# Kernel optimization log

Measured on AMD Instinct MI355X. Metric: run time of the kernel, lower is better.

Reference implementation:

```python
import jax, jax.numpy as jnp
import numpy as np

GS = 8        # grid_size
MARGIN = 1.0
LAMBDA = 1.0
BIG = 5.0     # mask penalty added to similarity matrix


def _bilinear(desc, coords):
    # desc: (c,h,w); coords: (n,2) as (y,x) in descriptor pixel space
    c, h, w = desc.shape
    y = jnp.clip(coords[:, 0], 0.0, h - 1.0)
    x = jnp.clip(coords[:, 1], 0.0, w - 1.0)
    y0 = jnp.floor(y); x0 = jnp.floor(x)
    y1 = jnp.minimum(y0 + 1.0, h - 1.0)
    x1 = jnp.minimum(x0 + 1.0, w - 1.0)
    wy = y - y0; wx = x - x0
    y0i = y0.astype(jnp.int32); y1i = y1.astype(jnp.int32)
    x0i = x0.astype(jnp.int32); x1i = x1.astype(jnp.int32)
    v00 = desc[:, y0i, x0i]; v01 = desc[:, y0i, x1i]
    v10 = desc[:, y1i, x0i]; v11 = desc[:, y1i, x1i]
    out = (v00 * (1 - wy) * (1 - wx) + v01 * (1 - wy) * wx
           + v10 * wy * (1 - wx) + v11 * wy * wx)
    return out.T  # (n,c)


def _forward(desc1, desc2, homo12, w_vis_mask1, score2):
    b, cdim, hc, wc = desc1.shape
    flat = hc * wc
    H, W = score2.shape[2], score2.shape[3]
    dt = desc1.dtype

    gy, gx = jnp.meshgrid(jnp.arange(hc, dtype=dt), jnp.arange(wc, dtype=dt), indexing='ij')
    # corner coordinate grid in image pixel space, (x,y) order
    coo1 = jnp.stack([gx * GS, gy * GS], -1).reshape(-1, 2)          # (flat,2)
    homog = jnp.concatenate([coo1, jnp.ones((flat, 1), dt)], -1)     # (flat,3)
    wpts = jnp.einsum('bij,nj->bni', homo12, homog)                  # warp by homography
    w_coo = wpts[..., :2] / (wpts[..., 2:3] + 1e-8)                  # (b,flat,2) (x,y)
    w_coo = w_coo[..., ::-1]                                         # swap to (y,x)

    # sample desc2 at warped coords (descriptor pixel space = image / GS)
    w_desc1 = jax.vmap(_bilinear)(desc2, w_coo / GS)                 # (b,flat,c)

    # center coordinate grid of desc2 cells, (y,x)
    coo2 = jnp.stack([gy * GS + GS / 2, gx * GS + GS / 2], -1).reshape(-1, 2)
    d2 = jnp.sum((w_coo[:, :, None, :] - coo2[None, None, :, :]) ** 2, -1)  # (b,flat,flat)
    ul = jnp.argmin(d2, -1)                                          # (b,flat)
    ur = jnp.where(ul + 1 >= flat, ul, ul + 1)
    ll = jnp.where(ul + wc >= flat, ul, ul + wc)
    lr = jnp.where(ll + 1 >= flat, ll, ll + 1)
    ids = jnp.stack([ul, ur, ll, lr], -1)                            # (b,flat,4)
    bi = jnp.arange(b)[:, None, None]
    ni = jnp.arange(flat)[None, :, None]
    neigh = jnp.zeros((b, flat, flat), dt).at[bi, ni, ids].set(1.0)

    # cell visible only if every pixel in the GSxGS cell is visible
    vis = w_vis_mask1.reshape(b, hc, GS, wc, GS).all(axis=(2, 4)).reshape(b, 1, flat)

    d1f = desc1.reshape(b, cdim, flat).transpose(0, 2, 1)            # (b,flat,c)
    d2f = desc2.reshape(b, cdim, flat).transpose(0, 2, 1)
    sim = 2.0 - 2.0 * jnp.einsum('bnc,bmc->bnm', d1f, d2f)           # inv similarity
    sim = sim + neigh * BIG + (1.0 - vis.astype(dt)) * BIG

    wv = ((w_coo[..., 0] >= 0) & (w_coo[..., 0] < H)
          & (w_coo[..., 1] >= 0) & (w_coo[..., 1] < W)).astype(dt)   # (b,flat)

    pos = 2.0 - 2.0 * jnp.sum(d1f * w_desc1, -1)                     # (b,flat)
    neg = jnp.min(sim, -1)
    l = jnp.maximum(pos - neg + MARGIN, 0.0) ** 2 * wv
    return jnp.sum(l) / jnp.sum(wv) * LAMBDA


def setup_inputs() -> dict:
    key = jax.random.key(0)
    k1, k2, k3, k4, k5 = jax.random.split(key, 5)
    b, c, H, W = 2, 256, 512, 512
    hc, wc = H // GS, W // GS
    d1 = jax.random.normal(k1, (b, c, hc, wc), jnp.float32)
    d1 = d1 / (jnp.linalg.norm(d1, axis=1, keepdims=True) + 1e-8)
    d2 = jax.random.normal(k2, (b, c, hc, wc), jnp.float32)
    d2 = d2 / (jnp.linalg.norm(d2, axis=1, keepdims=True) + 1e-8)
    homo12 = jnp.eye(3, dtype=jnp.float32)[None].repeat(b, 0) \
        + 1e-3 * jax.random.normal(k3, (b, 3, 3), jnp.float32)
    w_vis_mask1 = jax.random.uniform(k4, (b, 1, H, W)) > 0.02
    score2 = jax.random.uniform(k5, (b, 1, H, W), jnp.float32)
    return {"desc1": d1, "desc2": d2, "homo12": homo12,
            "w_vis_mask1": w_vis_mask1, "score2": score2}


def reference(desc1, desc2, homo12, w_vis_mask1, score2):
    return _forward(desc1, desc2, homo12, w_vis_mask1, score2)
```

## Files before the change

### kernel.cpp

```cpp
#include <hip/hip_runtime.h>

typedef __attribute__((ext_vector_type(8))) short s16x8;
typedef __attribute__((ext_vector_type(4))) float f32x4;
typedef __attribute__((ext_vector_type(4))) unsigned short u16x4;

#define FLAT 4096
#define CDIM 256
#define NB 2

#define OFF_D1T  0u
#define OFF_D2T  4194304u
#define OFF_PARTIAL 8388608u
#define OFF_POS  9437184u
#define OFF_WV   9469952u
#define OFF_VIS  9502720u
#define OFF_QUAD 9535488u
#define OFF_RED  9666560u
#define OFF_END  9667072u

__device__ __forceinline__ size_t t16_off(int R, int lane) {
  return (size_t)(R >> 4) * 4096 + ((lane >> 3) * 512) + (((lane >> 1) & 3) * 128) +
         ((R & 15) * 8) + ((lane & 1) * 4);
}

__device__ __forceinline__ float bf2f(unsigned short u) {
  return __uint_as_float(((unsigned)u) << 16);
}
__device__ __forceinline__ unsigned short f2bf(float v) {
  unsigned u = __float_as_uint(v);
  return (unsigned short)((u + 0x7FFFu + ((u >> 16) & 1u)) >> 16);
}
__device__ __forceinline__ void async_g2l(const void* g, void* l) {
  __builtin_amdgcn_global_load_lds(
      (const __attribute__((address_space(1))) unsigned int*)g,
      (__attribute__((address_space(3))) unsigned int*)l,
      16, 0, 0);
}

__global__ void k_initvis(const void* __restrict__ mask, float* __restrict__ vispen) {
  int tid = threadIdx.x;
  int idx = blockIdx.x * 256 + tid;
  __shared__ int sflag;
  if (tid < 64) {
    const unsigned* mw = (const unsigned*)mask;
    int odd = 0;
#pragma unroll
    for (int t = 0; t < 16; ++t) {
      unsigned w = mw[tid * 16 + t];
      odd += (w > 1u && w != 0x3F800000u) ? 1 : 0;
    }
#pragma unroll
    for (int d = 32; d >= 1; d >>= 1) odd += __shfl_xor(odd, d, 64);
    if (tid == 0) sflag = (odd > 16) ? 1 : 0;
  }
  __syncthreads();
  int b = idx >> 12, m = idx & 4095;
  int i = m >> 6, j = m & 63;
  bool ok = true;
  if (sflag) {
    const unsigned char* p = (const unsigned char*)mask + (size_t)b * 262144 + (size_t)(i * 8) * 512 + j * 8;
#pragma unroll
    for (int dy = 0; dy < 8; ++dy) {
      const unsigned* q = (const unsigned*)(p + (size_t)dy * 512);
      unsigned w0 = q[0], w1 = q[1];
      unsigned z0 = (w0 - 0x01010101u) & ~w0 & 0x80808080u;
      unsigned z1 = (w1 - 0x01010101u) & ~w1 & 0x80808080u;
      if (z0 | z1) ok = false;
    }
  } else {
    const unsigned* p = (const unsigned*)mask + (size_t)b * 262144 + (size_t)(i * 8) * 512 + j * 8;
#pragma unroll
    for (int dy = 0; dy < 8; ++dy) {
      const uint4* q = (const uint4*)(p + (size_t)dy * 512);
      uint4 u0 = q[0], u1 = q[1];
      if (!(u0.x && u0.y && u0.z && u0.w && u1.x && u1.y && u1.z && u1.w)) ok = false;
    }
  }
  vispen[idx] = ok ? 0.f : 5.f;
}

__global__ __launch_bounds__(256) void k_convert(const float* __restrict__ desc1,
                                                 const float* __restrict__ desc2,
                                                 unsigned short* __restrict__ d1T,
                                                 unsigned short* __restrict__ d2T) {
  __shared__ __align__(16) unsigned ldsw[64 * 128];
  int b = blockIdx.z, which = blockIdx.y;
  const float* src = (which ? desc2 : desc1) + (size_t)b * CDIM * FLAT;
  unsigned short* dst = (which ? d2T : d1T) + (size_t)b * FLAT * CDIM;
  int n0 = blockIdx.x * 64;
  int tid = threadIdx.x, wv = tid >> 6, lane = tid & 63;

  const float* s0 = src + n0 + lane;
#pragma unroll 2
  for (int r = 0; r < 64; r += 8) {
    int c0 = wv * 64 + r;
    float v[8];
#pragma unroll
    for (int t = 0; t < 8; ++t) v[t] = s0[(size_t)(c0 + t) * FLAT];
    unsigned pk[4];
#pragma unroll
    for (int t = 0; t < 4; ++t) pk[t] = (unsigned)f2bf(v[2 * t]) | ((unsigned)f2bf(v[2 * t + 1]) << 16);
    int pg = (c0 >> 3) ^ (lane & 31);
    *(uint4*)(ldsw + lane * 128 + pg * 4) = make_uint4(pk[0], pk[1], pk[2], pk[3]);
  }
  __syncthreads();
  int n = wv * 16 + (lane & 15);
#pragma unroll 2
  for (int it = 0; it < 8; ++it) {
    int g = it * 4 + (lane >> 4);
    uint4 d = *(const uint4*)(ldsw + n * 128 + ((g ^ (n & 31)) * 4));
    *(uint4*)(dst + ((size_t)(n0 >> 4) + wv) * 4096 + it * 512 + lane * 8) = d;
  }
}

__global__ void k_setup(const float* __restrict__ homo, const unsigned short* __restrict__ d1T,
                        const unsigned short* __restrict__ d2T, float* __restrict__ pos,
                        float* __restrict__ wv, int4* __restrict__ quads) {
  int b = blockIdx.z;
  int tid = threadIdx.x;
  int wid = tid >> 6, lane = tid & 63;
  int n = blockIdx.x * 4 + wid;
  int i = n >> 6, j = n & 63;
  const float* Hm = homo + b * 9;
  float x = (float)(j * 8), y = (float)(i * 8);
  float den = Hm[6] * x + Hm[7] * y + Hm[8] + 1e-8f;
  float wxc = (Hm[0] * x + Hm[1] * y + Hm[2]) / den;
  float wyc = (Hm[3] * x + Hm[4] * y + Hm[5]) / den;

  float vv = (wyc >= 0.f && wyc < 512.f && wxc >= 0.f && wxc < 512.f) ? 1.f : 0.f;

  int ic = min(63, max(0, (int)floorf(wyc * 0.125f)));
  int jc = min(63, max(0, (int)floorf(wxc * 0.125f)));
  int ul = ic * 64 + jc;
  int ur = (ul + 1 >= FLAT) ? ul : ul + 1;
  int ll = (ul + 64 >= FLAT) ? ul : ul + 64;
  int lr = (ll + 1 >= FLAT) ? ll : ll + 1;

  float cy = fminf(fmaxf(wyc * 0.125f, 0.f), 63.f);
  float cx = fminf(fmaxf(wxc * 0.125f, 0.f), 63.f);
  float y0 = floorf(cy), x0 = floorf(cx);
  float y1 = fminf(y0 + 1.f, 63.f), x1 = fminf(x0 + 1.f, 63.f);
  float fy = cy - y0, fx = cx - x0;
  float w00 = (1.f - fy) * (1.f - fx), w01 = (1.f - fy) * fx;
  float w10 = fy * (1.f - fx), w11 = fy * fx;
  int m00 = (int)y0 * 64 + (int)x0;
  int m01 = (int)y0 * 64 + (int)x1;
  int m10 = (int)y1 * 64 + (int)x0;
  int m11 = (int)y1 * 64 + (int)x1;

  size_t base = (size_t)b * FLAT * CDIM;
  u16x4 a   = *(const u16x4*)(d1T + base + t16_off(n, lane));
  u16x4 v00 = *(const u16x4*)(d2T + base + t16_off(m00, lane));
  u16x4 v01 = *(const u16x4*)(d2T + base + t16_off(m01, lane));
  u16x4 v10 = *(const u16x4*)(d2T + base + t16_off(m10, lane));
  u16x4 v11 = *(const u16x4*)(d2T + base + t16_off(m11, lane));
  float s = 0.f;
#pragma unroll
  for (int t = 0; t < 4; ++t) {
    float vt = w00 * bf2f(v00[t]) + w01 * bf2f(v01[t]) + w10 * bf2f(v10[t]) + w11 * bf2f(v11[t]);
    s += bf2f(a[t]) * vt;
  }
#pragma unroll
  for (int d = 32; d >= 1; d >>= 1) s += __shfl_xor(s, d, 64);
  if (lane == 0) {
    int idx = b * FLAT + n;
    pos[idx] = 2.f - 2.f * s;
    wv[idx] = vv;
    quads[idx] = make_int4(ul, ur, ll, lr);
  }
}

__global__ __launch_bounds__(256, 3) void k_gemm(const unsigned short* __restrict__ d1T,
                                                 const unsigned short* __restrict__ d2T,
                                                 const int4* __restrict__ quads,
                                                 const float* __restrict__ vispen,
                                                 float* __restrict__ partial) {
  __shared__ __align__(16) char lds[3][16384];
  int lin = blockIdx.x;
  int id = (lin & 7) * 256 + (lin >> 3);
  int b = id >> 10;
  int mn = id & 1023;
  int m0 = (mn & 31) << 7;
  int n0 = (mn >> 5) << 7;
  int tid = threadIdx.x;
  int wid = tid >> 6, lane = tid & 63;
  int wr = wid >> 1, wc = wid & 1;
  int lg = lane >> 4, ll16 = lane & 15;

  const unsigned short* Ab = d1T + (size_t)b * FLAT * CDIM;
  const unsigned short* Bb = d2T + (size_t)b * FLAT * CDIM;

  const unsigned short* srcq[4];
  int ldsoff[4];
#pragma unroll
  for (int q = 0; q < 4; ++q) {
    int idx = wid * 4 + q;
    int isA = idx < 8;
    int s = idx & 7;
    int rg = (((isA ? n0 : m0)) >> 4) + s;
    srcq[q] = (isA ? Ab : Bb) + (size_t)rg * 4096 + lane * 8;
    ldsoff[q] = (isA ? 0 : 8192) + s * 1024;
  }

  f32x4 acc[4][4] = {};

#define STAGE(t, p)                                            \
  {                                                            \
    _Pragma("unroll") for (int q = 0; q < 4; ++q)              \
        async_g2l(srcq[q] + (t) * 512, &lds[p][ldsoff[q]]);    \
  }

#define KSTEP(T, BUF, WN)                                                          \
  {                                                                                \
    asm volatile("s_waitcnt vmcnt(" #WN ")" ::: "memory");                         \
    __builtin_amdgcn_s_barrier();                                                  \
    const char* base_ = lds[BUF];                                                  \
    s16x8 af[4], bf[4];                                                            \
    _Pragma("unroll") for (int mi = 0; mi < 4; ++mi)                               \
        af[mi] = *(const s16x8*)(base_ + (wr * 4 + mi) * 1024 + lane * 16);        \
    _Pragma("unroll") for (int ni = 0; ni < 4; ++ni)                               \
        bf[ni] = *(const s16x8*)(base_ + 8192 + (wc * 4 + ni) * 1024 + lane * 16); \
    _Pragma("unroll") for (int mi = 0; mi < 4; ++mi)                               \
      _Pragma("unroll") for (int ni = 0; ni < 4; ++ni)                             \
          acc[mi][ni] =                                                            \
              __builtin_amdgcn_mfma_f32_16x16x32_bf16(af[mi], bf[ni], acc[mi][ni], 0, 0, 0); \
    asm volatile("s_waitcnt lgkmcnt(0)" ::: "memory");                             \
    __builtin_amdgcn_s_barrier();                                                  \
    if ((T) < 5) STAGE((T) + 3, ((T) + 3) % 3);                                    \
  }

  STAGE(0, 0);
  STAGE(1, 1);
  STAGE(2, 2);
  KSTEP(0, 0, 8) KSTEP(1, 1, 8) KSTEP(2, 2, 8) KSTEP(3, 0, 8)
  KSTEP(4, 1, 8) KSTEP(5, 2, 8) KSTEP(6, 0, 4) KSTEP(7, 1, 0)
#undef KSTEP
#undef STAGE

  const int4* qB = quads + b * FLAT;
  const float* vB = vispen + b * FLAT;
  float* red = (float*)lds;
  float pv[4];
#pragma unroll
  for (int ni = 0; ni < 4; ++ni) pv[ni] = vB[m0 + wc * 64 + ni * 16 + ll16];
#pragma unroll
  for (int mi = 0; mi < 4; ++mi) {
    int rowBase = wr * 64 + mi * 16 + lg * 4;
    float rm[4] = {1e30f, 1e30f, 1e30f, 1e30f};
    int4 q0 = qB[n0 + rowBase + 0];
    int4 q1 = qB[n0 + rowBase + 1];
    int4 q2 = qB[n0 + rowBase + 2];
    int4 q3 = qB[n0 + rowBase + 3];
#pragma unroll
    for (int ni = 0; ni < 4; ++ni) {
      int gm = m0 + wc * 64 + ni * 16 + ll16;
      f32x4 a = acc[mi][ni];
      float v0 = 2.f - 2.f * a[0] + pv[ni] + ((gm == q0.x || gm == q0.y || gm == q0.z || gm == q0.w) ? 5.f : 0.f);
      float v1 = 2.f - 2.f * a[1] + pv[ni] + ((gm == q1.x || gm == q1.y || gm == q1.z || gm == q1.w) ? 5.f : 0.f);
      float v2 = 2.f - 2.f * a[2] + pv[ni] + ((gm == q2.x || gm == q2.y || gm == q2.z || gm == q2.w) ? 5.f : 0.f);
      float v3 = 2.f - 2.f * a[3] + pv[ni] + ((gm == q3.x || gm == q3.y || gm == q3.z || gm == q3.w) ? 5.f : 0.f);
      rm[0] = fminf(rm[0], v0);
      rm[1] = fminf(rm[1], v1);
      rm[2] = fminf(rm[2], v2);
      rm[3] = fminf(rm[3], v3);
    }
#pragma unroll
    for (int r = 0; r < 4; ++r) {
      float v = rm[r];
#pragma unroll
      for (int d = 1; d < 16; d <<= 1) v = fminf(v, __shfl_xor(v, d, 64));
      if (ll16 == 0) red[(rowBase + r) * 2 + wc] = v;
    }
  }
  __syncthreads();
  if ((wid & 1) == 0) {
    int row = wr * 64 + lane;
    float v = fminf(red[row * 2], red[row * 2 + 1]);
    partial[((size_t)(b * 32 + (m0 >> 7))) * FLAT + n0 + row] = v;
  }
}

__global__ void k_redfin(const float* __restrict__ partial, const float* __restrict__ pos,
                         const float* __restrict__ wv, double* __restrict__ part) {
  int tid = threadIdx.x;
  int idx = blockIdx.x * 256 + tid;
  int wid = tid >> 6, lane = tid & 63;
  int b = idx >> 12, nl = idx & 4095;
  const float* ps = partial + (size_t)b * 32 * FLAT + nl;
  float neg = 1e30f;
#pragma unroll
  for (int s = 0; s < 32; ++s) neg = fminf(neg, ps[(size_t)s * FLAT]);
  float p = pos[idx], w = wv[idx];
  float t = fmaxf(p - neg + 1.f, 0.f);
  double aL = (double)(t * t) * (double)w;
  double aW = (double)w;
#pragma unroll
  for (int d = 32; d >= 1; d >>= 1) {
    aL += __shfl_xor(aL, d, 64);
    aW += __shfl_xor(aW, d, 64);
  }
  __shared__ double red[8];
  if (lane == 0) { red[wid * 2] = aL; red[wid * 2 + 1] = aW; }
  __syncthreads();
  if (tid == 0) {
    double L = 0.0, W = 0.0;
#pragma unroll
    for (int u = 0; u < 4; ++u) { L += red[u * 2]; W += red[u * 2 + 1]; }
    part[blockIdx.x * 2] = L;
    part[blockIdx.x * 2 + 1] = W;
  }
}

__global__ void k_fin2(const double* __restrict__ part, float* __restrict__ out) {
  int tid = threadIdx.x;
  double L = 0.0, W = 0.0;
  if (tid < 32) { L = part[2 * tid]; W = part[2 * tid + 1]; }
#pragma unroll
  for (int d = 16; d >= 1; d >>= 1) {
    L += __shfl_xor(L, d, 64);
    W += __shfl_xor(W, d, 64);
  }
  if (tid == 0) out[0] = (float)(L / W);
}

extern "C" void kernel_launch(void* const* d_in, const int* in_sizes, int n_in,
                              void* d_out, int out_size, void* d_ws, size_t ws_size,
                              hipStream_t stream) {
  if (ws_size < OFF_END) return;
  const float* desc1 = (const float*)d_in[0];
  const float* desc2 = (const float*)d_in[1];
  const float* homo = (const float*)d_in[2];
  const void* mask = d_in[3];

  char* ws = (char*)d_ws;
  unsigned short* d1T = (unsigned short*)(ws + OFF_D1T);
  unsigned short* d2T = (unsigned short*)(ws + OFF_D2T);
  float* partial = (float*)(ws + OFF_PARTIAL);
  float* pos = (float*)(ws + OFF_POS);
  float* wv = (float*)(ws + OFF_WV);
  float* vispen = (float*)(ws + OFF_VIS);
  int4* quads = (int4*)(ws + OFF_QUAD);
  double* part = (double*)(ws + OFF_RED);
  float* out = (float*)d_out;

  k_initvis<<<dim3(32), dim3(256), 0, stream>>>(mask, vispen);
  k_convert<<<dim3(64, 2, 2), dim3(256), 0, stream>>>(desc1, desc2, d1T, d2T);
  k_setup<<<dim3(1024, 1, 2), dim3(256), 0, stream>>>(homo, d1T, d2T, pos, wv, quads);
  k_gemm<<<dim3(2048), dim3(256), 0, stream>>>(d1T, d2T, quads, vispen, partial);
  k_redfin<<<dim3(32), dim3(256), 0, stream>>>(partial, pos, wv, part);
  k_fin2<<<dim3(1), dim3(64), 0, stream>>>(part, out);
}
```

Measured before the change: 59.35 us.

## Merge prologue kernels, enlarge GEMM tile to 256 rows, fuse final reduction

Merges the mask-penalty and bf16 transpose kernels into one launch and folds the final scalar reduction into k_redfin using an atomic last-block counter. This removes two kernel launches. The GEMM now uses 512-thread blocks covering 256 n-rows by 128 m-columns, so B tiles are shared across more rows and fewer blocks are launched. The cost is more LDS per block (72KB), a different occupancy target, and an epilogue that must now map 8 waves correctly onto the wider tile.

```diff
diff --git a/kernel.cpp b/kernel.cpp
--- a/kernel.cpp
+++ b/kernel.cpp
@@ -16,7 +16,8 @@
 #define OFF_VIS  9502720u
 #define OFF_QUAD 9535488u
 #define OFF_RED  9666560u
-#define OFF_END  9667072u
+#define OFF_CNT  9667072u
+#define OFF_END  9667328u
 
 __device__ __forceinline__ size_t t16_off(int R, int lane) {
   return (size_t)(R >> 4) * 4096 + ((lane >> 3) * 512) + (((lane >> 1) & 3) * 128) +
@@ -37,79 +38,83 @@
       16, 0, 0);
 }
 
-__global__ void k_initvis(const void* __restrict__ mask, float* __restrict__ vispen) {
+__global__ __launch_bounds__(256) void k_pre(const float* __restrict__ desc1,
+                                             const float* __restrict__ desc2,
+                                             unsigned short* __restrict__ d1T,
+                                             unsigned short* __restrict__ d2T,
+                                             const void* __restrict__ mask,
+                                             float* __restrict__ vispen,
+                                             unsigned* __restrict__ cnt) {
+  __shared__ __align__(16) unsigned ldsw[64 * 128];
+  int bid = blockIdx.x;
   int tid = threadIdx.x;
-  int idx = blockIdx.x * 256 + tid;
-  __shared__ int sflag;
-  if (tid < 64) {
-    const unsigned* mw = (const unsigned*)mask;
-    int odd = 0;
-#pragma unroll
-    for (int t = 0; t < 16; ++t) {
-      unsigned w = mw[tid * 16 + t];
-      odd += (w > 1u && w != 0x3F800000u) ? 1 : 0;
-    }
-#pragma unroll
-    for (int d = 32; d >= 1; d >>= 1) odd += __shfl_xor(odd, d, 64);
-    if (tid == 0) sflag = (odd > 16) ? 1 : 0;
-  }
-  __syncthreads();
-  int b = idx >> 12, m = idx & 4095;
-  int i = m >> 6, j = m & 63;
-  bool ok = true;
-  if (sflag) {
-    const unsigned char* p = (const unsigned char*)mask + (size_t)b * 262144 + (size_t)(i * 8) * 512 + j * 8;
-#pragma unroll
-    for (int dy = 0; dy < 8; ++dy) {
-      const unsigned* q = (const unsigned*)(p + (size_t)dy * 512);
-      unsigned w0 = q[0], w1 = q[1];
-      unsigned z0 = (w0 - 0x01010101u) & ~w0 & 0x80808080u;
-      unsigned z1 = (w1 - 0x01010101u) & ~w1 & 0x80808080u;
-      if (z0 | z1) ok = false;
+  if (bid < 256) {
+    int x = bid & 63, which = (bid >> 6) & 1, b = bid >> 7;
+    const float* src = (which ? desc2 : desc1) + (size_t)b * CDIM * FLAT;
+    unsigned short* dst = (which ? d2T : d1T) + (size_t)b * FLAT * CDIM;
+    int n0 = x * 64;
+    int wv = tid >> 6, lane = tid & 63;
+    const float* s0 = src + n0 + lane;
+#pragma unroll 2
+    for (int r = 0; r < 64; r += 8) {
+      int c0 = wv * 64 + r;
+      float v[8];
+#pragma unroll
+      for (int t = 0; t < 8; ++t) v[t] = s0[(size_t)(c0 + t) * FLAT];
+      unsigned pk[4];
+#pragma unroll
+      for (int t = 0; t < 4; ++t) pk[t] = (unsigned)f2bf(v[2 * t]) | ((unsigned)f2bf(v[2 * t + 1]) << 16);
+      int pg = (c0 >> 3) ^ (lane & 31);
+      *(uint4*)(ldsw + lane * 128 + pg * 4) = make_uint4(pk[0], pk[1], pk[2], pk[3]);
+    }
+    __syncthreads();
+    int n = wv * 16 + (lane & 15);
+#pragma unroll 2
+    for (int it = 0; it < 8; ++it) {
+      int g = it * 4 + (lane >> 4);
+      uint4 d = *(const uint4*)(ldsw + n * 128 + ((g ^ (n & 31)) * 4));
+      *(uint4*)(dst + ((size_t)(n0 >> 4) + wv) * 4096 + it * 512 + lane * 8) = d;
     }
   } else {
-    const unsigned* p = (const unsigned*)mask + (size_t)b * 262144 + (size_t)(i * 8) * 512 + j * 8;
-#pragma unroll
-    for (int dy = 0; dy < 8; ++dy) {
-      const uint4* q = (const uint4*)(p + (size_t)dy * 512);
-      uint4 u0 = q[0], u1 = q[1];
-      if (!(u0.x && u0.y && u0.z && u0.w && u1.x && u1.y && u1.z && u1.w)) ok = false;
-    }
-  }
-  vispen[idx] = ok ? 0.f : 5.f;
-}
-
-__global__ __launch_bounds__(256) void k_convert(const float* __restrict__ desc1,
-                                                 const float* __restrict__ desc2,
-                                                 unsigned short* __restrict__ d1T,
-                                                 unsigned short* __restrict__ d2T) {
-  __shared__ __align__(16) unsigned ldsw[64 * 128];
-  int b = blockIdx.z, which = blockIdx.y;
-  const float* src = (which ? desc2 : desc1) + (size_t)b * CDIM * FLAT;
-  unsigned short* dst = (which ? d2T : d1T) + (size_t)b * FLAT * CDIM;
-  int n0 = blockIdx.x * 64;
-  int tid = threadIdx.x, wv = tid >> 6, lane = tid & 63;
-
-  const float* s0 = src + n0 + lane;
-#pragma unroll 2
-  for (int r = 0; r < 64; r += 8) {
-    int c0 = wv * 64 + r;
-    float v[8];
-#pragma unroll
-    for (int t = 0; t < 8; ++t) v[t] = s0[(size_t)(c0 + t) * FLAT];
-    unsigned pk[4];
-#pragma unroll
-    for (int t = 0; t < 4; ++t) pk[t] = (unsigned)f2bf(v[2 * t]) | ((unsigned)f2bf(v[2 * t + 1]) << 16);
-    int pg = (c0 >> 3) ^ (lane & 31);
-    *(uint4*)(ldsw + lane * 128 + pg * 4) = make_uint4(pk[0], pk[1], pk[2], pk[3]);
-  }
-  __syncthreads();
-  int n = wv * 16 + (lane & 15);
-#pragma unroll 2
-  for (int it = 0; it < 8; ++it) {
-    int g = it * 4 + (lane >> 4);
-    uint4 d = *(const uint4*)(ldsw + n * 128 + ((g ^ (n & 31)) * 4));
-    *(uint4*)(dst + ((size_t)(n0 >> 4) + wv) * 4096 + it * 512 + lane * 8) = d;
+    int idx = (bid - 256) * 256 + tid;
+    if (idx == 0) *cnt = 0u;
+    __shared__ int sflag;
+    if (tid < 64) {
+      const unsigned* mw = (const unsigned*)mask;
+      int odd = 0;
+#pragma unroll
+      for (int t = 0; t < 16; ++t) {
+        unsigned w = mw[tid * 16 + t];
+        odd += (w > 1u && w != 0x3F800000u) ? 1 : 0;
+      }
+#pragma unroll
+      for (int d = 32; d >= 1; d >>= 1) odd += __shfl_xor(odd, d, 64);
+      if (tid == 0) sflag = (odd > 16) ? 1 : 0;
+    }
+    __syncthreads();
+    int b = idx >> 12, m = idx & 4095;
+    int i = m >> 6, j = m & 63;
+    bool ok = true;
+    if (sflag) {
+      const unsigned char* p = (const unsigned char*)mask + (size_t)b * 262144 + (size_t)(i * 8) * 512 + j * 8;
+#pragma unroll
+      for (int dy = 0; dy < 8; ++dy) {
+        const unsigned* q = (const unsigned*)(p + (size_t)dy * 512);
+        unsigned w0 = q[0], w1 = q[1];
+        unsigned z0 = (w0 - 0x01010101u) & ~w0 & 0x80808080u;
+        unsigned z1 = (w1 - 0x01010101u) & ~w1 & 0x80808080u;
+        if (z0 | z1) ok = false;
+      }
+    } else {
+      const unsigned* p = (const unsigned*)mask + (size_t)b * 262144 + (size_t)(i * 8) * 512 + j * 8;
+#pragma unroll
+      for (int dy = 0; dy < 8; ++dy) {
+        const uint4* q = (const uint4*)(p + (size_t)dy * 512);
+        uint4 u0 = q[0], u1 = q[1];
+        if (!(u0.x && u0.y && u0.z && u0.w && u1.x && u1.y && u1.z && u1.w)) ok = false;
+      }
+    }
+    vispen[idx] = ok ? 0.f : 5.f;
   }
 }
 
@@ -170,18 +175,18 @@
   }
 }
 
-__global__ __launch_bounds__(256, 3) void k_gemm(const unsigned short* __restrict__ d1T,
+__global__ __launch_bounds__(512, 4) void k_gemm(const unsigned short* __restrict__ d1T,
                                                  const unsigned short* __restrict__ d2T,
                                                  const int4* __restrict__ quads,
                                                  const float* __restrict__ vispen,
                                                  float* __restrict__ partial) {
-  __shared__ __align__(16) char lds[3][16384];
+  __shared__ __align__(16) char lds[3][24576];
   int lin = blockIdx.x;
-  int id = (lin & 7) * 256 + (lin >> 3);
-  int b = id >> 10;
-  int mn = id & 1023;
+  int id = (lin & 7) * 128 + (lin >> 3);
+  int b = id >> 9;
+  int mn = id & 511;
   int m0 = (mn & 31) << 7;
-  int n0 = (mn >> 5) << 7;
+  int n0 = (mn >> 5) << 8;
   int tid = threadIdx.x;
   int wid = tid >> 6, lane = tid & 63;
   int wr = wid >> 1, wc = wid & 1;
@@ -190,50 +195,50 @@
   const unsigned short* Ab = d1T + (size_t)b * FLAT * CDIM;
   const unsigned short* Bb = d2T + (size_t)b * FLAT * CDIM;
 
-  const unsigned short* srcq[4];
-  int ldsoff[4];
-#pragma unroll
-  for (int q = 0; q < 4; ++q) {
-    int idx = wid * 4 + q;
-    int isA = idx < 8;
-    int s = idx & 7;
+  const unsigned short* srcq[3];
+  int ldsoff[3];
+#pragma unroll
+  for (int q = 0; q < 3; ++q) {
+    int idx = wid * 3 + q;
+    int isA = idx < 16;
+    int s = isA ? idx : idx - 16;
     int rg = (((isA ? n0 : m0)) >> 4) + s;
     srcq[q] = (isA ? Ab : Bb) + (size_t)rg * 4096 + lane * 8;
-    ldsoff[q] = (isA ? 0 : 8192) + s * 1024;
+    ldsoff[q] = (isA ? 0 : 16384) + s * 1024;
   }
 
   f32x4 acc[4][4] = {};
 
 #define STAGE(t, p)                                            \
   {                                                            \
-    _Pragma("unroll") for (int q = 0; q < 4; ++q)              \
+    _Pragma("unroll") for (int q = 0; q < 3; ++q)              \
         async_g2l(srcq[q] + (t) * 512, &lds[p][ldsoff[q]]);    \
   }
 
-#define KSTEP(T, BUF, WN)                                                          \
-  {                                                                                \
-    asm volatile("s_waitcnt vmcnt(" #WN ")" ::: "memory");                         \
-    __builtin_amdgcn_s_barrier();                                                  \
-    const char* base_ = lds[BUF];                                                  \
-    s16x8 af[4], bf[4];                                                            \
-    _Pragma("unroll") for (int mi = 0; mi < 4; ++mi)                               \
-        af[mi] = *(const s16x8*)(base_ + (wr * 4 + mi) * 1024 + lane * 16);        \
-    _Pragma("unroll") for (int ni = 0; ni < 4; ++ni)                               \
-        bf[ni] = *(const s16x8*)(base_ + 8192 + (wc * 4 + ni) * 1024 + lane * 16); \
-    _Pragma("unroll") for (int mi = 0; mi < 4; ++mi)                               \
-      _Pragma("unroll") for (int ni = 0; ni < 4; ++ni)                             \
-          acc[mi][ni] =                                                            \
+#define KSTEP(T, WN)                                                                \
+  {                                                                                 \
+    asm volatile("s_waitcnt vmcnt(" #WN ")" ::: "memory");                          \
+    __builtin_amdgcn_s_barrier();                                                   \
+    const char* base_ = lds[(T) % 3];                                               \
+    s16x8 af[4], bf[4];                                                             \
+    _Pragma("unroll") for (int mi = 0; mi < 4; ++mi)                                \
+        af[mi] = *(const s16x8*)(base_ + (wr * 4 + mi) * 1024 + lane * 16);         \
+    _Pragma("unroll") for (int ni = 0; ni < 4; ++ni)                                \
+        bf[ni] = *(const s16x8*)(base_ + 16384 + (wc * 4 + ni) * 1024 + lane * 16); \
+    _Pragma("unroll") for (int mi = 0; mi < 4; ++mi)                                \
+      _Pragma("unroll") for (int ni = 0; ni < 4; ++ni)                              \
+          acc[mi][ni] =                                                             \
               __builtin_amdgcn_mfma_f32_16x16x32_bf16(af[mi], bf[ni], acc[mi][ni], 0, 0, 0); \
-    asm volatile("s_waitcnt lgkmcnt(0)" ::: "memory");                             \
-    __builtin_amdgcn_s_barrier();                                                  \
-    if ((T) < 5) STAGE((T) + 3, ((T) + 3) % 3);                                    \
+    asm volatile("s_waitcnt lgkmcnt(0)" ::: "memory");                              \
+    __builtin_amdgcn_s_barrier();                                                   \
+    if ((T) < 5) STAGE((T) + 3, ((T) + 3) % 3);                                     \
   }
 
   STAGE(0, 0);
   STAGE(1, 1);
   STAGE(2, 2);
-  KSTEP(0, 0, 8) KSTEP(1, 1, 8) KSTEP(2, 2, 8) KSTEP(3, 0, 8)
-  KSTEP(4, 1, 8) KSTEP(5, 2, 8) KSTEP(6, 0, 4) KSTEP(7, 1, 0)
+  KSTEP(0, 6) KSTEP(1, 6) KSTEP(2, 6) KSTEP(3, 6)
+  KSTEP(4, 6) KSTEP(5, 6) KSTEP(6, 3) KSTEP(7, 0)
 #undef KSTEP
 #undef STAGE
 
@@ -281,9 +286,11 @@
 }
 
 __global__ void k_redfin(const float* __restrict__ partial, const float* __restrict__ pos,
-                         const float* __restrict__ wv, double* __restrict__ part) {
+                         const float* __restrict__ wv, double* __restrict__ part,
+                         unsigned* __restrict__ cnt, float* __restrict__ out) {
   int tid = threadIdx.x;
-  int idx = blockIdx.x * 256 + tid;
+  int bid = blockIdx.x;
+  int idx = bid * 256 + tid;
   int wid = tid >> 6, lane = tid & 63;
   int b = idx >> 12, nl = idx & 4095;
   const float* ps = partial + (size_t)b * 32 * FLAT + nl;
@@ -300,27 +307,30 @@
     aW += __shfl_xor(aW, d, 64);
   }
   __shared__ double red[8];
+  __shared__ int lastFlag;
   if (lane == 0) { red[wid * 2] = aL; red[wid * 2 + 1] = aW; }
   __syncthreads();
   if (tid == 0) {
     double L = 0.0, W = 0.0;
 #pragma unroll
     for (int u = 0; u < 4; ++u) { L += red[u * 2]; W += red[u * 2 + 1]; }
-    part[blockIdx.x * 2] = L;
-    part[blockIdx.x * 2 + 1] = W;
-  }
-}
-
-__global__ void k_fin2(const double* __restrict__ part, float* __restrict__ out) {
-  int tid = threadIdx.x;
-  double L = 0.0, W = 0.0;
-  if (tid < 32) { L = part[2 * tid]; W = part[2 * tid + 1]; }
-#pragma unroll
-  for (int d = 16; d >= 1; d >>= 1) {
-    L += __shfl_xor(L, d, 64);
-    W += __shfl_xor(W, d, 64);
-  }
-  if (tid == 0) out[0] = (float)(L / W);
+    part[bid * 2] = L;
+    part[bid * 2 + 1] = W;
+    __threadfence();
+    unsigned old = atomicAdd(cnt, 1u);
+    lastFlag = (old == 31u) ? 1 : 0;
+  }
+  __syncthreads();
+  if (lastFlag && wid == 0) {
+    double L = 0.0, W = 0.0;
+    if (lane < 32) { L = part[2 * lane]; W = part[2 * lane + 1]; }
+#pragma unroll
+    for (int d = 16; d >= 1; d >>= 1) {
+      L += __shfl_xor(L, d, 64);
+      W += __shfl_xor(W, d, 64);
+    }
+    if (lane == 0) out[0] = (float)(L / W);
+  }
 }
 
 extern "C" void kernel_launch(void* const* d_in, const int* in_sizes, int n_in,
@@ -341,12 +351,11 @@
   float* vispen = (float*)(ws + OFF_VIS);
   int4* quads = (int4*)(ws + OFF_QUAD);
   double* part = (double*)(ws + OFF_RED);
+  unsigned* cnt = (unsigned*)(ws + OFF_CNT);
   float* out = (float*)d_out;
 
-  k_initvis<<<dim3(32), dim3(256), 0, stream>>>(mask, vispen);
-  k_convert<<<dim3(64, 2, 2), dim3(256), 0, stream>>>(desc1, desc2, d1T, d2T);
+  k_pre<<<dim3(288), dim3(256), 0, stream>>>(desc1, desc2, d1T, d2T, mask, vispen, cnt);
   k_setup<<<dim3(1024, 1, 2), dim3(256), 0, stream>>>(homo, d1T, d2T, pos, wv, quads);
-  k_gemm<<<dim3(2048), dim3(256), 0, stream>>>(d1T, d2T, quads, vispen, partial);
-  k_redfin<<<dim3(32), dim3(256), 0, stream>>>(partial, pos, wv, part);
-  k_fin2<<<dim3(1), dim3(64), 0, stream>>>(part, out);
-}
+  k_gemm<<<dim3(1024), dim3(512), 0, stream>>>(d1T, d2T, quads, vispen, partial);
+  k_redfin<<<dim3(32), dim3(256), 0, stream>>>(partial, pos, wv, part, cnt, out);
+}
```

Result: faster. 57.43 us (-3.2%).
